# Performance work log

Hardware: AMD Instinct MI355X
Metric: run time of the kernel (lower is better)

## Reference

```python
import jax, jax.numpy as jnp
import numpy as np

U = 256      # lstm_unit / embedding_fc_unit
V = 100000   # word vocab
WD = 300     # word embedding dim
PD = 64      # pos embedding dim
AD = 64      # action embedding dim
P = 50       # pos vocab
NA = 164     # 4 + 4*dep_num actions
B, T, K, L, S, A, DQ = 64, 128, 4, 128, 64, 64, 32
FORGET_BIAS = 1.0


def lstm_step(x, c, h, W, b):
    z = jnp.concatenate([x, h], -1) @ W + b
    i, j, f, o = jnp.split(z, 4, -1)
    nc = c * jax.nn.sigmoid(f + FORGET_BIAS) + jax.nn.sigmoid(i) * jnp.tanh(j)
    nh = jnp.tanh(nc) * jax.nn.sigmoid(o)
    return nc, nh


def run_lstm(xs, length, W, b):
    # xs: [B, L, D]; TF dynamic_rnn semantics: state frozen and output zeroed past length.
    Bn, Ln, _ = xs.shape
    u = W.shape[1] // 4
    def step(carry, tx):
        c, h = carry
        t, x = tx
        nc, nh = lstm_step(x, c, h, W, b)
        m = (t < length)[:, None]
        return (jnp.where(m, nc, c), jnp.where(m, nh, h)), jnp.where(m, nh, 0.0)
    init = (jnp.zeros((Bn, u), xs.dtype), jnp.zeros((Bn, u), xs.dtype))
    (cf, hf), outs = jax.lax.scan(step, init, (jnp.arange(Ln), jnp.swapaxes(xs, 0, 1)))
    return jnp.swapaxes(outs, 0, 1), (cf, hf)


def reverse_seq(xs, length):
    # tf.reverse_sequence: reverse first `length` steps, leave the rest in place.
    Ln = xs.shape[1]
    t = jnp.arange(Ln)[None, :]
    rev = jnp.where(t < length[:, None], length[:, None] - 1 - t, t)
    return jnp.take_along_axis(xs, rev[:, :, None], axis=1)


def forward(tree_word_id, tree_pos_id, token_word_id, token_pos_id, history_action_id,
            buff_top_id, deque_word_id, deque_pos_id, deque_length, children_order,
            stack_order, stack_length, token_length, history_action_length,
            word_emb, pos_emb, act_emb, wd_W, wd_b, tree_W, tree_b,
            stack0_W, stack0_b, stack1_W, stack1_b,
            fw0_W, fw0_b, bw0_W, bw0_b, fw1_W, fw1_b, bw1_W, bw1_b,
            act0_W, act0_b, act1_W, act1_b, dq0_W, dq0_b, dq1_W, dq1_b,
            fin_W, fin_b):
    Bn = tree_word_id.shape[0]

    def embed(wid, pid):
        e = jnp.concatenate([word_emb[wid], pos_emb[pid]], -1)
        return jax.nn.relu(e @ wd_W + wd_b)

    tree_e = embed(tree_word_id, tree_pos_id)       # [B, T, U]
    token_e = embed(token_word_id, token_pos_id)    # [B, L, U]
    deque_e = embed(deque_word_id, deque_pos_id)    # [B, DQ, U]
    hist_e = act_emb[history_action_id]             # [B, A, AD]

    # ---- tree LSTM over children structure ----
    Tn = tree_e.shape[1]
    Kn = children_order.shape[2]
    batch_col = jnp.arange(Bn)[:, None]
    H0 = jnp.zeros((Tn + 1, Bn, U), tree_e.dtype)
    C0 = jnp.zeros((Tn + 1, Bn, U), tree_e.dtype)

    def body(carry, i):
        H, C = carry
        idx = children_order[:, i]            # [B, K] indices into slots 0..i
        h = H[idx, batch_col]                 # [B, K, U]
        c = C[idx, batch_col]
        x = tree_e[:, i]                      # [B, U]
        hj = h.sum(1)
        ijo = jnp.concatenate([x, hj], -1) @ tree_W[:, :3 * U] + tree_b[:3 * U]
        xk = jnp.broadcast_to(x[:, None, :], (Bn, Kn, x.shape[-1]))
        f = jnp.concatenate([xk, h], -1) @ tree_W[:, 3 * U:] + tree_b[3 * U:]   # [B, K, U]
        ig, jg, og = jnp.split(ijo, 3, -1)
        nc = (c * jax.nn.sigmoid(f + FORGET_BIAS)).sum(1) + jax.nn.sigmoid(ig) * jnp.tanh(jg)
        nh = jnp.tanh(nc) * jax.nn.sigmoid(og)
        return (H.at[i + 1].set(nh), C.at[i + 1].set(nc)), None

    (H, _), _ = jax.lax.scan(body, (H0, C0), jnp.arange(Tn))
    stack_embedded = H[stack_order, batch_col]      # [B, S, U]

    # ---- stack LSTM (2-layer) ----
    o0, _ = run_lstm(stack_embedded, stack_length, stack0_W, stack0_b)
    _, (_, stack_h) = run_lstm(o0, stack_length, stack1_W, stack1_b)

    # ---- buff bi-LSTM (2 stacked bidirectional layers) ----
    fw0_o, _ = run_lstm(token_e, token_length, fw0_W, fw0_b)
    bw0_o, _ = run_lstm(reverse_seq(token_e, token_length), token_length, bw0_W, bw0_b)
    bw0_o = reverse_seq(bw0_o, token_length)
    x1 = jnp.concatenate([fw0_o, bw0_o], -1)
    fw1_o, (_, fw1_h) = run_lstm(x1, token_length, fw1_W, fw1_b)
    bw1_o, _ = run_lstm(reverse_seq(x1, token_length), token_length, bw1_W, bw1_b)
    bw1_o = reverse_seq(bw1_o, token_length)
    bidx = jnp.arange(Bn)
    fw_top = fw1_o[bidx, buff_top_id]
    bw_top = bw1_o[bidx, buff_top_id]
    bw_bottom = bw1_o[bidx, token_length - 1]
    buff_out = jnp.concatenate([fw1_h - fw_top, bw_top - bw_bottom], -1)

    # ---- action LSTM (2-layer) ----
    a0, _ = run_lstm(hist_e, history_action_length, act0_W, act0_b)
    _, (_, act_h) = run_lstm(a0, history_action_length, act1_W, act1_b)

    # ---- deque LSTM (2-layer) ----
    d0, _ = run_lstm(deque_e, deque_length, dq0_W, dq0_b)
    _, (_, dq_h) = run_lstm(d0, deque_length, dq1_W, dq1_b)

    feat = jnp.concatenate([stack_h, buff_out, act_h, dq_h], -1)   # [B, 5U]
    return jax.nn.relu(feat @ fin_W + fin_b)


def setup_inputs():
    key = jax.random.key(0)
    ks = jax.random.split(key, 48)
    r = lambda i, shape: jax.random.normal(ks[i], shape, jnp.float32) * 0.05
    ri = lambda i, shape, hi: jax.random.randint(ks[i], shape, 0, hi)
    inp = {}
    inp['tree_word_id'] = ri(0, (B, T), V)
    inp['tree_pos_id'] = ri(1, (B, T), P)
    inp['token_word_id'] = ri(2, (B, L), V)
    inp['token_pos_id'] = ri(3, (B, L), P)
    inp['history_action_id'] = ri(4, (B, A), NA)
    inp['buff_top_id'] = ri(5, (B,), L // 2)
    inp['deque_word_id'] = ri(6, (B, DQ), V)
    inp['deque_pos_id'] = ri(7, (B, DQ), P)
    inp['deque_length'] = jax.random.randint(ks[8], (B,), 1, DQ + 1)
    co = ri(9, (B, T, K), T)
    # a node may only reference already-computed children slots (<= step index)
    inp['children_order'] = jnp.minimum(co, jnp.arange(T)[None, :, None])
    inp['stack_order'] = ri(10, (B, S), T + 1)
    inp['stack_length'] = jax.random.randint(ks[11], (B,), 1, S + 1)
    inp['token_length'] = jax.random.randint(ks[12], (B,), L // 2, L + 1)
    inp['history_action_length'] = jax.random.randint(ks[13], (B,), 1, A + 1)
    inp['word_emb'] = r(14, (V, WD))
    inp['pos_emb'] = r(15, (P, PD))
    inp['act_emb'] = r(16, (NA, AD))
    inp['wd_W'] = r(17, (WD + PD, U)); inp['wd_b'] = jnp.zeros((U,))
    inp['tree_W'] = r(18, (2 * U, 4 * U)); inp['tree_b'] = jnp.zeros((4 * U,))
    inp['stack0_W'] = r(19, (2 * U, 4 * U)); inp['stack0_b'] = jnp.zeros((4 * U,))
    inp['stack1_W'] = r(20, (2 * U, 4 * U)); inp['stack1_b'] = jnp.zeros((4 * U,))
    inp['fw0_W'] = r(21, (2 * U, 4 * U)); inp['fw0_b'] = jnp.zeros((4 * U,))
    inp['bw0_W'] = r(22, (2 * U, 4 * U)); inp['bw0_b'] = jnp.zeros((4 * U,))
    inp['fw1_W'] = r(23, (3 * U, 4 * U)); inp['fw1_b'] = jnp.zeros((4 * U,))
    inp['bw1_W'] = r(24, (3 * U, 4 * U)); inp['bw1_b'] = jnp.zeros((4 * U,))
    inp['act0_W'] = r(25, (AD + U, 4 * U)); inp['act0_b'] = jnp.zeros((4 * U,))
    inp['act1_W'] = r(26, (2 * U, 4 * U)); inp['act1_b'] = jnp.zeros((4 * U,))
    inp['dq0_W'] = r(27, (2 * U, 4 * U)); inp['dq0_b'] = jnp.zeros((4 * U,))
    inp['dq1_W'] = r(28, (2 * U, 4 * U)); inp['dq1_b'] = jnp.zeros((4 * U,))
    inp['fin_W'] = r(29, (5 * U, NA)); inp['fin_b'] = jnp.zeros((NA,))
    return inp


def reference(tree_word_id, tree_pos_id, token_word_id, token_pos_id, history_action_id,
              buff_top_id, deque_word_id, deque_pos_id, deque_length, children_order,
              stack_order, stack_length, token_length, history_action_length,
              word_emb, pos_emb, act_emb, wd_W, wd_b, tree_W, tree_b,
              stack0_W, stack0_b, stack1_W, stack1_b,
              fw0_W, fw0_b, bw0_W, bw0_b, fw1_W, fw1_b, bw1_W, bw1_b,
              act0_W, act0_b, act1_W, act1_b, dq0_W, dq0_b, dq1_W, dq1_b,
              fin_W, fin_b):
    return forward(tree_word_id, tree_pos_id, token_word_id, token_pos_id, history_action_id,
                   buff_top_id, deque_word_id, deque_pos_id, deque_length, children_order,
                   stack_order, stack_length, token_length, history_action_length,
                   word_emb, pos_emb, act_emb, wd_W, wd_b, tree_W, tree_b,
                   stack0_W, stack0_b, stack1_W, stack1_b,
                   fw0_W, fw0_b, bw0_W, bw0_b, fw1_W, fw1_b, bw1_W, bw1_b,
                   act0_W, act0_b, act1_W, act1_b, dq0_W, dq0_b, dq1_W, dq1_b,
                   fin_W, fin_b)
```

## Files before the change

### kernel.cpp

```cpp
#include <hip/hip_runtime.h>
#include <hip/hip_bf16.h>
#include <hip/hip_fp16.h>
#include <cstdint>

#define BB   64
#define TT   128
#define KK   4
#define LL   128
#define SS   64
#define AA   64
#define DQN  32
#define UU   256
#define NAOUT 164
#define WDIM 300
#define PDIM 64
#define ADIM 64

#define OFF_TREE 0
#define OFF_S0   512
#define OFF_S1   1024
#define OFF_FW0  1536
#define OFF_BW0  2048
#define OFF_FW1  2560
#define OFF_BW1  3328
// ... 313 lines not shown
        const float fsum = c0 * sigm(fx + f0) + c1 * sigm(fx + f1)
                         + c2 * sigm(fx + f2) + c3 * sigm(fx + f3);
        const float nc = fsum + sigm(zi) * tanhf(zj);
        const float nh = tanhf(nc) * sigm(zo);
        __syncthreads();
        H[((size_t)(i + 1) * BB + b) * UU + u] = nh;
        C[((size_t)(i + 1) * BB + b) * UU + u] = nc;
    }
}

template<bool F32>
__device__ void run_token_l0_f4(int b, const P& p, float* smem, bool is_bw) {
    const int u = threadIdx.x;
    float* s_xh = smem;
    const int len = p.token_length[b];
    const float4* __restrict__ Wp = p.pkf + (size_t)(is_bw ? OFF_BW0 : OFF_FW0) * 256 + u;
    const float4 bz = load_bias4<F32>(is_bw ? p.bw0_b : p.fw0_b, u);

    float c0 = 0.f;
    s_xh[256 + u] = 0.f;
    for (int t = 0; t < len; ++t) {
        const int row = is_bw ? (len - 1 - t) : t;
        s_xh[u] = bf2f(p.token_e[((size_t)b * LL + row) * UU + u]);
        __syncthreads();
        const float nh = lstm_step_f4<512>(Wp, bz, s_xh, c0);
        p.x1[((size_t)b * LL + row) * 512 + (is_bw ? 256 : 0) + u] = f2bf(nh);
        __syncthreads();
        s_xh[256 + u] = nh;
    }
}

template<bool F32>
__device__ void run_act_dq_f4(int b, const P& p, float* smem) {
    const int u = threadIdx.x;
    float* s_xh0 = smem;
    float* s_xh1 = smem + 512;

    {
        const int len = p.history_action_length[b];
        const float4* __restrict__ W0 = p.pkf + (size_t)OFF_ACT0 * 256 + u;
        const float4* __restrict__ W1 = p.pkf + (size_t)OFF_ACT1 * 256 + u;
        const float4 bz0 = load_bias4<F32>(p.act0_b, u);
        const float4 bz1 = load_bias4<F32>(p.act1_b, u);
        float ca0 = 0.f, ca1 = 0.f, h1last = 0.f;
        s_xh0[ADIM + u] = 0.f;
        s_xh1[256 + u]  = 0.f;
        for (int t = 0; t < len; ++t) {
            const int aid = p.history_action_id[b * AA + t];
            if (u < ADIM) s_xh0[u] = ld1<F32>(p.act_emb, (size_t)aid * ADIM + u);
            __syncthreads();
            const float nh0 = lstm_step_f4<320>(W0, bz0, s_xh0, ca0);
            __syncthreads();
            s_xh0[ADIM + u] = nh0;
            s_xh1[u]        = nh0;
            __syncthreads();
            const float nh1 = lstm_step_f4<512>(W1, bz1, s_xh1, ca1);
            __syncthreads();
            s_xh1[256 + u] = nh1;
            h1last = nh1;
        }
        p.act_h[b * UU + u] = h1last;
    }
    __syncthreads();
    {
        const int len = p.deque_length[b];
        const float4* __restrict__ W0 = p.pkf + (size_t)OFF_DQ0 * 256 + u;
        const float4* __restrict__ W1 = p.pkf + (size_t)OFF_DQ1 * 256 + u;
        const float4 bz0 = load_bias4<F32>(p.dq0_b, u);
        const float4 bz1 = load_bias4<F32>(p.dq1_b, u);
        float cd0 = 0.f, cd1 = 0.f, h1last = 0.f;
        s_xh0[256 + u] = 0.f;
        s_xh1[256 + u] = 0.f;
        for (int t = 0; t < len; ++t) {
            s_xh0[u] = bf2f(p.deque_e[((size_t)b * DQN + t) * UU + u]);
            __syncthreads();
            const float nh0 = lstm_step_f4<512>(W0, bz0, s_xh0, cd0);
            __syncthreads();
            s_xh0[256 + u] = nh0;
            s_xh1[u]       = nh0;
            __syncthreads();
            const float nh1 = lstm_step_f4<512>(W1, bz1, s_xh1, cd1);
            __syncthreads();
            s_xh1[256 + u] = nh1;
            h1last = nh1;
        }
        p.dq_h[b * UU + u] = h1last;
    }
}

__global__ __launch_bounds__(256) void phase1_fb_kernel(P p) {
    __shared__ __align__(16) float smem[1536];
    const bool f32 = (p.flag[0] == 1);
    const int chain = blockIdx.x & 3;
    const int b     = blockIdx.x >> 2;
    if (f32) {
        if (chain == 0)      run_tree_f4<true>(b, p, smem);
        else if (chain == 1) run_token_l0_f4<true>(b, p, smem, false);
        else if (chain == 2) run_token_l0_f4<true>(b, p, smem, true);
        else                 run_act_dq_f4<true>(b, p, smem);
    } else {
        if (chain == 0)      run_tree_f4<false>(b, p, smem);
        else if (chain == 1) run_token_l0_f4<false>(b, p, smem, false);
        else if (chain == 2) run_token_l0_f4<false>(b, p, smem, true);
        else                 run_act_dq_f4<false>(b, p, smem);
    }
}

template<bool F32>
__device__ void run_stack_f4(int b, const P& p, float* smem) {
    const int u = threadIdx.x;
    float* s_xh0 = smem;
    float* s_xh1 = smem + 512;
    const int len = p.stack_length[b];
    const float4* __restrict__ W0 = p.pkf + (size_t)OFF_S0 * 256 + u;
    const float4* __restrict__ W1 = p.pkf + (size_t)OFF_S1 * 256 + u;
    const float4 bz0 = load_bias4<F32>(p.stack0_b, u);
    const float4 bz1 = load_bias4<F32>(p.stack1_b, u);
    float cs0 = 0.f, cs1 = 0.f, h1last = 0.f;
    s_xh0[256 + u] = 0.f;
    s_xh1[256 + u] = 0.f;
    for (int t = 0; t < len; ++t) {
        const int so = p.stack_order[b * SS + t];
        s_xh0[u] = p.H[((size_t)so * BB + b) * UU + u];
        __syncthreads();
        const float nh0 = lstm_step_f4<512>(W0, bz0, s_xh0, cs0);
        __syncthreads();
        s_xh0[256 + u] = nh0;
        s_xh1[u]       = nh0;
        __syncthreads();
        const float nh1 = lstm_step_f4<512>(W1, bz1, s_xh1, cs1);
        __syncthreads();
        s_xh1[256 + u] = nh1;
        h1last = nh1;
    }
    p.stack_h[b * UU + u] = h1last;
}

template<bool F32>
__device__ void run_token_l1_f4(int b, const P& p, float* smem, bool is_bw) {
    const int u = threadIdx.x;
    float* s_xh = smem;
    const int len  = p.token_length[b];
    const int btop = p.buff_top_id[b];
    const float4* __restrict__ Wp = p.pkf + (size_t)(is_bw ? OFF_BW1 : OFF_FW1) * 256 + u;
    const float4 bz = load_bias4<F32>(is_bw ? p.bw1_b : p.fw1_b, u);

    float c1 = 0.f, hlast = 0.f;
    s_xh[512 + u] = 0.f;
    for (int t = 0; t < len; ++t) {
        const int row = is_bw ? (len - 1 - t) : t;
        const ushort_t* xr = p.x1 + ((size_t)b * LL + row) * 512;
        s_xh[u]       = bf2f(xr[u]);
        s_xh[256 + u] = bf2f(xr[256 + u]);
        __syncthreads();
        const float nh = lstm_step_f4<768>(Wp, bz, s_xh, c1);
        if (!is_bw) {
            if (t == btop) p.fw_top[b * UU + u] = nh;
        } else {
            if (t == 0)              p.bw_bottom[b * UU + u] = nh;
            if (t == len - 1 - btop) p.bw_top[b * UU + u]    = nh;
        }
        __syncthreads();
        s_xh[512 + u] = nh;
        hlast = nh;
    }
    if (!is_bw) p.fw1_h[b * UU + u] = hlast;
}

__global__ __launch_bounds__(256) void phase2_fb_kernel(P p) {
    __shared__ __align__(16) float smem[1024];
    const bool f32 = (p.flag[0] == 1);
    const int chain = blockIdx.x % 3;
    const int b     = blockIdx.x / 3;
    if (f32) {
        if (chain == 0)      run_stack_f4<true>(b, p, smem);
        else if (chain == 1) run_token_l1_f4<true>(b, p, smem, false);
        else                 run_token_l1_f4<true>(b, p, smem, true);
    } else {
        if (chain == 0)      run_stack_f4<false>(b, p, smem);
        else if (chain == 1) run_token_l1_f4<false>(b, p, smem, false);
        else                 run_token_l1_f4<false>(b, p, smem, true);
    }
}

template<bool F32, int R>
__device__ void xpre_compute(const void* __restrict__ W, const void* __restrict__ bias,
                             uint2* __restrict__ zx, int n0,
                             const float* __restrict__ s_xf, const ushort_t* __restrict__ s_xb) {
    const int u = threadIdx.x;
    const float4 bz = load_bias4<F32>(bias, u);
    for (int c = 0; c < 32; c += 8) {
        float4 acc[8];
        #pragma unroll
        for (int n = 0; n < 8; ++n) acc[n] = bz;
        for (int r0 = 0; r0 < R; r0 += 8) {
            float4 w[8];
            #pragma unroll
            for (int k = 0; k < 8; ++k) {
                const size_t ro = (size_t)(r0 + k) * 1024;
                w[k] = make_float4(ld1<F32>(W, ro + u),
                                   ld1<F32>(W, ro + 256 + u),
                                   ld1<F32>(W, ro + 512 + u),
                                   ld1<F32>(W, ro + 768 + u));
            }
            #pragma unroll
            for (int n = 0; n < 8; ++n) {
                float xv[8];
                #pragma unroll
                for (int k = 0; k < 8; ++k)
                    xv[k] = (R == 512) ? bf2f(s_xb[(size_t)(c + n) * 512 + r0 + k])
                                       : s_xf[(size_t)(c + n) * R + r0 + k];
                #pragma unroll
                for (int k = 0; k < 8; ++k) {
                    acc[n].x = fmaf(xv[k], w[k].x, acc[n].x);
                    acc[n].y = fmaf(xv[k], w[k].y, acc[n].y);
                    acc[n].z = fmaf(xv[k], w[k].z, acc[n].z);
                    acc[n].w = fmaf(xv[k], w[k].w, acc[n].w);
                }
            }
        }
        #pragma unroll
        for (int n = 0; n < 8; ++n) {
            uint2 v;
            v.x = pack2h(acc[n].x, acc[n].y);
            v.y = pack2h(acc[n].z, acc[n].w);
            zx[(size_t)(n0 + c + n) * 256 + u] = v;
        }
    }
}

template<bool F32, int STAGE>
__device__ void xpre_impl(const P& p, char* s_raw) {
    float*    s_xf = reinterpret_cast<float*>(s_raw);
    ushort_t* s_xb = reinterpret_cast<ushort_t*>(s_raw);
    const int blk = blockIdx.x;
    const int tid = threadIdx.x;

    const void* W; const void* bias; uint2* zx; int R; int kind; int n0;
    if (STAGE == 0) {
        if (blk < 256)      { W=p.fw0_W;  bias=p.fw0_b;  zx=p.zxA; R=256; kind=0; n0=blk*32; }
        else if (blk < 512) { W=p.bw0_W;  bias=p.bw0_b;  zx=p.zxB; R=256; kind=0; n0=(blk-256)*32; }
        else if (blk < 640) { W=p.act0_W; bias=p.act0_b; zx=p.zxC; R=64;  kind=3; n0=(blk-512)*32; }
        else                { W=p.dq0_W;  bias=p.dq0_b;  zx=p.zxD; R=256; kind=1; n0=(blk-640)*32; }
    } else if (STAGE == 1) {
        if (blk < 256)      { W=p.fw1_W;    bias=p.fw1_b;    zx=p.zxA; R=512; kind=2; n0=blk*32; }
        else if (blk < 512) { W=p.bw1_W;    bias=p.bw1_b;    zx=p.zxB; R=512; kind=2; n0=(blk-256)*32; }
        else if (blk < 640) { W=p.stack0_W; bias=p.stack0_b; zx=p.zxS; R=256; kind=4; n0=(blk-512)*32; }
        else if (blk < 768) { W=p.act1_W;   bias=p.act1_b;   zx=p.zxC; R=256; kind=5; n0=(blk-640)*32; }
        else                { W=p.dq1_W;    bias=p.dq1_b;    zx=p.zxD; R=256; kind=6; n0=(blk-768)*32; }
    } else {
        W=p.stack1_W; bias=p.stack1_b; zx=p.zxS; R=256; kind=7; n0=blk*32;
    }

    if (kind == 0 || kind == 1) {
        const ushort_t* src = (kind == 0 ? p.token_e : p.deque_e) + (size_t)n0 * 256;
        for (int i = tid; i < 32 * 256; i += 256) s_xf[i] = bf2f(src[i]);
    } else if (kind == 2) {
        const ushort_t* src = p.x1 + (size_t)n0 * 512;
        for (int i = tid; i < 32 * 512; i += 256) s_xb[i] = src[i];
    } else if (kind == 3) {
        const int b = n0 >> 6, t0 = n0 & 63;
        for (int i = tid; i < 32 * 64; i += 256) {
            const int t = t0 + (i >> 6), r = i & 63;
            int aid = p.history_action_id[b * AA + t];
            aid = aid < 0 ? 0 : (aid > NAOUT - 1 ? NAOUT - 1 : aid);
            s_xf[i] = ld1<F32>(p.act_emb, (size_t)aid * ADIM + r);
        }
    } else if (kind == 4) {
        const int b = n0 >> 6, t0 = n0 & 63;
        for (int i = tid; i < 32 * 256; i += 256) {
            const int t = t0 + (i >> 8), r = i & 255;
            int so = p.stack_order[b * SS + t];
            so = so < 0 ? 0 : (so > TT ? TT : so);
            s_xf[i] = p.H[((size_t)so * BB + b) * UU + r];
        }
    } else {
        const float* src = (kind == 5 ? p.a0_seq : kind == 6 ? p.d0_seq : p.s0_seq)
                         + (size_t)n0 * 256;
        for (int i = tid; i < 32 * 256; i += 256) s_xf[i] = src[i];
    }
    __syncthreads();

    if (R == 512)      xpre_compute<F32, 512>(W, bias, zx, n0, s_xf, s_xb);
    else if (R == 256) xpre_compute<F32, 256>(W, bias, zx, n0, s_xf, s_xb);
    else               xpre_compute<F32, 64 >(W, bias, zx, n0, s_xf, s_xb);
}

__global__ __launch_bounds__(256) void xpre0_kernel(P p) {
    __shared__ __align__(16) char s_raw[32768];
    if (p.flag[0] == 1) xpre_impl<true, 0>(p, s_raw);
    else                xpre_impl<false, 0>(p, s_raw);
}
__global__ __launch_bounds__(256) void xpre1_kernel(P p) {
    __shared__ __align__(16) char s_raw[32768];
    if (p.flag[0] == 1) xpre_impl<true, 1>(p, s_raw);
    else                xpre_impl<false, 1>(p, s_raw);
}
__global__ __launch_bounds__(256) void xpre2_kernel(P p) {
    __shared__ __align__(16) char s_raw[32768];
    if (p.flag[0] == 1) xpre_impl<true, 2>(p, s_raw);
    else                xpre_impl<false, 2>(p, s_raw);
}

template<bool F32>
__device__ void p1_impl(const P& p, float* smem) {
    const int chain = blockIdx.x >> 6;
    const int b     = blockIdx.x & 63;
    if (chain == 0) { run_tree_f4<F32>(b, p, smem); return; }

    const int u = threadIdx.x;
    float* s_h = smem;
    float c = 0.f;
    s_h[u] = 0.f;
    __syncthreads();

    if (chain == 1 || chain == 2) {
        const bool bw = (chain == 2);
        const int len = p.token_length[b];
        const float4* __restrict__ Wh = p.pkf + (size_t)(bw ? PKH_BW0 : PKH_FW0) * 256 + u;
        const uint2* zx = bw ? p.zxB : p.zxA;
        for (int t = 0; t < len; ++t) {
            const int row = bw ? (len - 1 - t) : t;
            const float4 bz = zx_load(zx, (size_t)b * LL + row, u);
            const float nh = lstm_step_f4<256>(Wh, bz, s_h, c);
            p.x1[((size_t)b * LL + row) * 512 + (bw ? 256 : 0) + u] = f2bf(nh);
            __syncthreads();
            s_h[u] = nh;
            __syncthreads();
        }
    } else if (chain == 3) {
        const int len = p.history_action_length[b];
        const float4* __restrict__ Wh = p.pkf + (size_t)PKH_ACT0 * 256 + u;
        for (int t = 0; t < len; ++t) {
            const float4 bz = zx_load(p.zxC, (size_t)b * AA + t, u);
            const float nh = lstm_step_f4<256>(Wh, bz, s_h, c);
            p.a0_seq[((size_t)b * AA + t) * UU + u] = nh;
            __syncthreads();
            s_h[u] = nh;
            __syncthreads();
        }
    } else {
        const int len = p.deque_length[b];
        const float4* __restrict__ Wh = p.pkf + (size_t)PKH_DQ0 * 256 + u;
        for (int t = 0; t < len; ++t) {
            const float4 bz = zx_load(p.zxD, (size_t)b * DQN + t, u);
            const float nh = lstm_step_f4<256>(Wh, bz, s_h, c);
            p.d0_seq[((size_t)b * DQN + t) * UU + u] = nh;
            __syncthreads();
            s_h[u] = nh;
            __syncthreads();
        }
    }
}

__global__ __launch_bounds__(256) void p1_kernel(P p) {
    __shared__ __align__(16) float smem[1536];
    if (p.flag[0] == 1) p1_impl<true>(p, smem);
    else                p1_impl<false>(p, smem);
}

template<bool F32>
__device__ void p2_impl(const P& p, float* smem) {
    const int chain = blockIdx.x >> 6;
    const int b     = blockIdx.x & 63;
    const int u = threadIdx.x;
    float* s_h = smem;
    float c = 0.f;
    s_h[u] = 0.f;
    __syncthreads();

    if (chain == 0) {
        const int len  = p.token_length[b];
        const int btop = p.buff_top_id[b];
        const float4* __restrict__ Wh = p.pkf + (size_t)PKH_FW1 * 256 + u;
        float hlast = 0.f;
        for (int t = 0; t < len; ++t) {
            const float4 bz = zx_load(p.zxA, (size_t)b * LL + t, u);
            const float nh = lstm_step_f4<256>(Wh, bz, s_h, c);
            if (t == btop) p.fw_top[b * UU + u] = nh;
            __syncthreads();
            s_h[u] = nh;
            __syncthreads();
            hlast = nh;
        }
        p.fw1_h[b * UU + u] = hlast;
    } else if (chain == 1) {
        const int len  = p.token_length[b];
        const int btop = p.buff_top_id[b];
        const float4* __restrict__ Wh = p.pkf + (size_t)PKH_BW1 * 256 + u;
        for (int t = 0; t < len; ++t) {
            const int row = len - 1 - t;
            const float4 bz = zx_load(p.zxB, (size_t)b * LL + row, u);
            const float nh = lstm_step_f4<256>(Wh, bz, s_h, c);
            if (t == 0)              p.bw_bottom[b * UU + u] = nh;
            if (t == len - 1 - btop) p.bw_top[b * UU + u]    = nh;
            __syncthreads();
            s_h[u] = nh;
            __syncthreads();
        }
    } else if (chain == 2) {
        const int len = p.stack_length[b];
        const float4* __restrict__ Wh = p.pkf + (size_t)PKH_S0 * 256 + u;
        for (int t = 0; t < len; ++t) {
            const float4 bz = zx_load(p.zxS, (size_t)b * SS + t, u);
            const float nh = lstm_step_f4<256>(Wh, bz, s_h, c);
            p.s0_seq[((size_t)b * SS + t) * UU + u] = nh;
            __syncthreads();
            s_h[u] = nh;
            __syncthreads();
        }
    } else if (chain == 3) {
        const int len = p.history_action_length[b];
        const float4* __restrict__ Wh = p.pkf + (size_t)PKH_ACT1 * 256 + u;
        float hlast = 0.f;
        for (int t = 0; t < len; ++t) {
            const float4 bz = zx_load(p.zxC, (size_t)b * AA + t, u);
            const float nh = lstm_step_f4<256>(Wh, bz, s_h, c);
            __syncthreads();
            s_h[u] = nh;
            __syncthreads();
            hlast = nh;
        }
        p.act_h[b * UU + u] = hlast;
    } else {
        const int len = p.deque_length[b];
        const float4* __restrict__ Wh = p.pkf + (size_t)PKH_DQ1 * 256 + u;
        float hlast = 0.f;
        for (int t = 0; t < len; ++t) {
            const float4 bz = zx_load(p.zxD, (size_t)b * DQN + t, u);
            const float nh = lstm_step_f4<256>(Wh, bz, s_h, c);
            __syncthreads();
            s_h[u] = nh;
            __syncthreads();
            hlast = nh;
        }
        p.dq_h[b * UU + u] = hlast;
    }
}

__global__ __launch_bounds__(256) void p2_kernel(P p) {
    __shared__ __align__(16) float smem[256];
    if (p.flag[0] == 1) p2_impl<true>(p, smem);
    else                p2_impl<false>(p, smem);
}

template<bool F32>
__device__ void p3_impl(const P& p, float* smem) {
    const int b = blockIdx.x;
    const int u = threadIdx.x;
    float* s_h = smem;
    float c = 0.f;
    s_h[u] = 0.f;
    __syncthreads();
    const int len = p.stack_length[b];
    const float4* __restrict__ Wh = p.pkf + (size_t)PKH_S1 * 256 + u;
    float hlast = 0.f;
    for (int t = 0; t < len; ++t) {
        const float4 bz = zx_load(p.zxS, (size_t)b * SS + t, u);
        const float nh = lstm_step_f4<256>(Wh, bz, s_h, c);
        __syncthreads();
        s_h[u] = nh;
        __syncthreads();
        hlast = nh;
    }
    p.stack_h[b * UU + u] = hlast;
}

__global__ __launch_bounds__(256) void p3_kernel(P p) {
    __shared__ __align__(16) float smem[256];
    if (p.flag[0] == 1) p3_impl<true>(p, smem);
    else                p3_impl<false>(p, smem);
}

template<bool F32>
__device__ __forceinline__ void st_out(void* out, int i, float v) {
    if constexpr (F32) reinterpret_cast<float*>(out)[i] = v;
    else               reinterpret_cast<__hip_bfloat16*>(out)[i] = __float2bfloat16(v);
}

template<bool F32>
__device__ void final_impl(const P& p, void* out, float* s_f) {
    const int b = blockIdx.x;
    const int u = threadIdx.x;
    s_f[u]        = p.stack_h[b * UU + u];
    s_f[256 + u]  = p.fw1_h[b * UU + u] - p.fw_top[b * UU + u];
    s_f[512 + u]  = p.bw_top[b * UU + u] - p.bw_bottom[b * UU + u];
    s_f[768 + u]  = p.act_h[b * UU + u];
    s_f[1024 + u] = p.dq_h[b * UU + u];
    __syncthreads();
    if (u < NAOUT) {
        float acc = ld1<F32>(p.fin_b, u);
        for (int r = 0; r < 1280; ++r)
            acc = fmaf(s_f[r], ld1<F32>(p.fin_W, (size_t)r * NAOUT + u), acc);
        acc = fmaxf(acc, 0.f);
        st_out<F32>(out, b * NAOUT + u, acc);
    }
    if (b == 0 && u == 0) {
        const uint_t POIS = 0xAAAAAAAAu;
        const uint_t* te = reinterpret_cast<const uint_t*>(p.tree_e);
        const uint_t* x1 = reinterpret_cast<const uint_t*>(p.x1);
        const uint_t* sh = reinterpret_cast<const uint_t*>(p.stack_h);
        bool te_p = true, x1_p = true;
        for (int i = 0; i < 8; ++i) { te_p &= (te[i] == POIS); x1_p &= (x1[i] == POIS); }
        bool sh_p = (sh[0] == POIS) && (sh[1] == POIS);
        float sent = 0.f;
        if (te_p)      sent = 3000.f;
        else if (x1_p) sent = 4000.f;
        else if (sh_p) sent = 5000.f;
        else if (*reinterpret_cast<const uint_t*>(p.flag) == POIS) sent = 6000.f;
        if (sent > 0.f) st_out<F32>(out, 0, sent);
    }
}

__global__ __launch_bounds__(256) void final_kernel(P p, void* out) {
    __shared__ __align__(16) float s_f[1280];
    if (p.flag[0] == 1) final_impl<true>(p, out, s_f);
    else                final_impl<false>(p, out, s_f);
}

extern "C" void kernel_launch(void* const* d_in, const int* in_sizes, int n_in,
                              void* d_out, int out_size, void* d_ws, size_t ws_size,
                              hipStream_t stream) {
    if (n_in != 43) {
        sentinel_kernel<<<1, 64, 0, stream>>>(d_out, 9000.f + (float)n_in);
        return;
    }
    if (out_size != NAOUT * BB) {
        sentinel_kernel<<<1, 64, 0, stream>>>(d_out, 8000.f);
        return;
    }

    P p;
    p.tree_word_id          = (const int*)d_in[0];
    p.tree_pos_id           = (const int*)d_in[1];
    p.token_word_id         = (const int*)d_in[2];
    p.token_pos_id          = (const int*)d_in[3];
    p.history_action_id     = (const int*)d_in[4];
    p.buff_top_id           = (const int*)d_in[5];
    p.deque_word_id         = (const int*)d_in[6];
    p.deque_pos_id          = (const int*)d_in[7];
    p.deque_length          = (const int*)d_in[8];
    p.children_order        = (const int*)d_in[9];
    p.stack_order           = (const int*)d_in[10];
    p.stack_length          = (const int*)d_in[11];
    p.token_length          = (const int*)d_in[12];
    p.history_action_length = (const int*)d_in[13];
    p.word_emb = d_in[14];
    p.pos_emb  = d_in[15];
    p.act_emb  = d_in[16];
    p.wd_W     = d_in[17];
    p.wd_b     = d_in[18];
    p.tree_W   = d_in[19];
    p.tree_b   = d_in[20];
    p.stack0_W = d_in[21];
    p.stack0_b = d_in[22];
    p.stack1_W = d_in[23];
    p.stack1_b = d_in[24];
    p.fw0_W    = d_in[25];
    p.fw0_b    = d_in[26];
    p.bw0_W    = d_in[27];
    p.bw0_b    = d_in[28];
    p.fw1_W    = d_in[29];
    p.fw1_b    = d_in[30];
    p.bw1_W    = d_in[31];
    p.bw1_b    = d_in[32];
    p.act0_W   = d_in[33];
    p.act0_b   = d_in[34];
    p.act1_W   = d_in[35];
    p.act1_b   = d_in[36];
    p.dq0_W    = d_in[37];
    p.dq0_b    = d_in[38];
    p.dq1_W    = d_in[39];
    p.dq1_b    = d_in[40];
    p.fin_W    = d_in[41];
    p.fin_b    = d_in[42];

    char* base = (char*)d_ws;

    size_t off = 0;
    p.flag = (int*)(base + off);           off += 256;
    p.stack_h   = (float*)(base + off);    off += (size_t)BB * UU * 4;
    p.fw1_h     = (float*)(base + off);    off += (size_t)BB * UU * 4;
    p.fw_top    = (float*)(base + off);    off += (size_t)BB * UU * 4;
    p.bw_top    = (float*)(base + off);    off += (size_t)BB * UU * 4;
    p.bw_bottom = (float*)(base + off);    off += (size_t)BB * UU * 4;
    p.act_h     = (float*)(base + off);    off += (size_t)BB * UU * 4;
    p.dq_h      = (float*)(base + off);    off += (size_t)BB * UU * 4;
    p.tree_e  = (float*)(base + off);      off += (size_t)BB * TT * UU * 4;
    p.token_e = (ushort_t*)(base + off);   off += (size_t)BB * LL * UU * 2;
    p.deque_e = (ushort_t*)(base + off);   off += (size_t)BB * DQN * UU * 2;
    p.x1      = (ushort_t*)(base + off);   off += (size_t)BB * LL * 512 * 2;
    p.a0_seq  = (float*)(base + off);      off += (size_t)BB * AA * UU * 4;
    p.d0_seq  = (float*)(base + off);      off += (size_t)BB * DQN * UU * 4;
    p.s0_seq  = (float*)(base + off);      off += (size_t)BB * SS * UU * 4;
    p.H       = (float*)(base + off);      off += (size_t)(TT + 1) * BB * UU * 4;
    p.C       = (float*)(base + off);      off += (size_t)(TT + 1) * BB * UU * 4;
    p.zxA     = (uint2*)(base + off);      off += (size_t)BB * LL * UU * 8;
    p.zxB     = (uint2*)(base + off);      off += (size_t)BB * LL * UU * 8;
    p.zxC     = (uint2*)(base + off);      off += (size_t)BB * AA * UU * 8;
    p.zxD     = (uint2*)(base + off);      off += (size_t)BB * DQN * UU * 8;
    p.zxS     = (uint2*)(base + off);      off += (size_t)BB * SS * UU * 8;
    p.pkf     = (float4*)(base + off);     off += (size_t)PK_ROWS_B * 256 * 16;
    const size_t planB_size = off;

    if (ws_size >= planB_size) {
        detect_kernel<<<1, 64, 0, stream>>>((const uint_t*)d_in[14], p.flag);
        pack_h_kernel<<<dim3(PK_ROWS_B), dim3(256), 0, stream>>>(p);
        embed_kernel<<<dim3(BB * TT + BB * LL + BB * DQN), dim3(256), 0, stream>>>(p);
        xpre0_kernel<<<dim3(704), dim3(256), 0, stream>>>(p);
        p1_kernel<<<dim3(5 * BB), dim3(256), 0, stream>>>(p);
        xpre1_kernel<<<dim3(832), dim3(256), 0, stream>>>(p);
        p2_kernel<<<dim3(5 * BB), dim3(256), 0, stream>>>(p);
        xpre2_kernel<<<dim3(128), dim3(256), 0, stream>>>(p);
        p3_kernel<<<dim3(BB), dim3(256), 0, stream>>>(p);
        final_kernel<<<dim3(BB), dim3(256), 0, stream>>>(p, d_out);
        return;
    }

    off = 0;
    p.flag = (int*)(base + off);           off += 16;
    p.stack_h   = (float*)(base + off);    off += (size_t)BB * UU * 4;
    p.fw1_h     = (float*)(base + off);    off += (size_t)BB * UU * 4;
    p.fw_top    = (float*)(base + off);    off += (size_t)BB * UU * 4;
    p.bw_top    = (float*)(base + off);    off += (size_t)BB * UU * 4;
    p.bw_bottom = (float*)(base + off);    off += (size_t)BB * UU * 4;
    p.act_h     = (float*)(base + off);    off += (size_t)BB * UU * 4;
    p.dq_h      = (float*)(base + off);    off += (size_t)BB * UU * 4;
    p.tree_e  = (float*)(base + off);      off += (size_t)BB * TT * UU * 4;
    p.token_e = (ushort_t*)(base + off);   off += (size_t)BB * LL * UU * 2;
    p.deque_e = (ushort_t*)(base + off);   off += (size_t)BB * DQN * UU * 2;
    p.x1      = (ushort_t*)(base + off);   off += (size_t)BB * LL * 512 * 2;
    p.H       = (float*)(base + off);      off += (size_t)(TT + 1) * BB * UU * 4;
    p.C       = (float*)(base + off);      off += (size_t)(TT + 1) * BB * UU * 4;
    p.pkf     = (float4*)(base + off);     off += (size_t)PK_ROWS_FB * 256 * 16;
    p.a0_seq = p.d0_seq = p.s0_seq = (float*)base;
    p.zxA = p.zxB = p.zxC = p.zxD = p.zxS = (uint2*)base;

    if (ws_size < off) {
        sentinel_kernel<<<1, 64, 0, stream>>>(d_out, 7000.f + (float)(ws_size >> 20));
        return;
    }

    detect_kernel<<<1, 64, 0, stream>>>((const uint_t*)d_in[14], p.flag);
    pack_fb_kernel<<<dim3(PK_ROWS_FB), dim3(256), 0, stream>>>(p);
    embed_kernel<<<dim3(BB * TT + BB * LL + BB * DQN), dim3(256), 0, stream>>>(p);
    phase1_fb_kernel<<<dim3(4 * BB), dim3(256), 0, stream>>>(p);
    phase2_fb_kernel<<<dim3(3 * BB), dim3(256), 0, stream>>>(p);
    final_kernel<<<dim3(BB), dim3(256), 0, stream>>>(p, d_out);
}
```

Before: 6.336 ms.

## Split recurrent LSTM matvec across four thread groups with 1024-thread blocks

The sequential LSTM recurrence kernels (tree, bidirectional, action, deque, stack chains) now use 1024 threads per block. Each group of 256 threads computes a 64-row (or 128-row for the tree) slice of the hidden-state matvec, and the partial sums are reduced through shared memory before the gate math. The goal is to shorten the per-step latency of the serial recurrence by spreading the weight loads and FMAs over four times as many threads. In exchange it adds a partial-sum shared buffer, an extra reduction step and barriers across 16 wavefronts, and it raises register and LDS pressure per block.

```diff
diff --git a/kernel.cpp b/kernel.cpp
--- a/kernel.cpp
+++ b/kernel.cpp
@@ -639,16 +639,209 @@
     else                xpre_impl<false, 2>(p, s_raw);
 }
 
+
+__device__ __forceinline__ float4 part64(const float4* __restrict__ W_u, int base,
+                                         const float* __restrict__ s_h) {
+    float4 acc = make_float4(0.f, 0.f, 0.f, 0.f);
+    for (int r0 = 0; r0 < 64; r0 += 8) {
+        float4 w[8];
+        #pragma unroll
+        for (int k = 0; k < 8; ++k) w[k] = W_u[(size_t)(base + r0 + k) * 256];
+        __builtin_amdgcn_sched_barrier(0);
+        #pragma unroll
+        for (int q = 0; q < 2; ++q) {
+            const float4 x4 = *reinterpret_cast<const float4*>(s_h + base + r0 + 4 * q);
+            const float xv[4] = {x4.x, x4.y, x4.z, x4.w};
+            #pragma unroll
+            for (int j = 0; j < 4; ++j) {
+                const float4 wv = w[4 * q + j];
+                acc.x = fmaf(xv[j], wv.x, acc.x);
+                acc.y = fmaf(xv[j], wv.y, acc.y);
+                acc.z = fmaf(xv[j], wv.z, acc.z);
+                acc.w = fmaf(xv[j], wv.w, acc.w);
+            }
+        }
+    }
+    return acc;
+}
+
+__device__ __forceinline__ float hstep(const float4* __restrict__ W_u,
+                                       const uint2* __restrict__ zx, size_t n,
+                                       float* s_h, float* s_pt,
+                                       float& c, int u, int rq) {
+    float4 bz = make_float4(0.f, 0.f, 0.f, 0.f);
+    if (rq == 0) bz = zx_load(zx, n, u);
+    const float4 acc = part64(W_u, rq << 6, s_h);
+    *reinterpret_cast<float4*>(s_pt + (((rq << 8) + u) << 2)) = acc;
+    __syncthreads();
+    float nh = 0.f;
+    if (rq == 0) {
+        const float4 P0 = *reinterpret_cast<const float4*>(s_pt + ((u)        << 2));
+        const float4 P1 = *reinterpret_cast<const float4*>(s_pt + ((256 + u)  << 2));
+        const float4 P2 = *reinterpret_cast<const float4*>(s_pt + ((512 + u)  << 2));
+        const float4 P3 = *reinterpret_cast<const float4*>(s_pt + ((768 + u)  << 2));
+        const float zi = bz.x + P0.x + P1.x + P2.x + P3.x;
+        const float zj = bz.y + P0.y + P1.y + P2.y + P3.y;
+        const float zf = bz.z + P0.z + P1.z + P2.z + P3.z;
+        const float zo = bz.w + P0.w + P1.w + P2.w + P3.w;
+        const float nc = c * sigm(zf) + sigm(zi) * tanhf(zj);
+        c = nc;
+        nh = tanhf(nc) * sigm(zo);
+    }
+    return nh;
+}
+
+template<bool F32>
+__device__ void run_tree_1024(int b, const P& p, float* smem) {
+    const int t = threadIdx.x;
+    const int u = t & 255, rq = t >> 8;
+    float* s_x  = smem;
+    float* s_hk = smem + 256;
+    float* s_pt = smem + 1280;
+    float* H = p.H;
+    float* C = p.C;
+    if (rq == 0) {
+        H[(size_t)b * UU + u] = 0.f;
+        C[(size_t)b * UU + u] = 0.f;
+    }
+    const float4* __restrict__ Wt = p.pkf + u;
+    const float4* __restrict__ Wh = Wt + (size_t)256 * 256;
+    const float bi = ld1<F32>(p.tree_b, u);
+    const float bj = ld1<F32>(p.tree_b, 256 + u);
+    const float bo = ld1<F32>(p.tree_b, 512 + u);
+    const float bf = ld1<F32>(p.tree_b, 768 + u) + 1.0f;
+    __syncthreads();
+
+    for (int i = 0; i < TT; ++i) {
+        const int* co = p.children_order + ((size_t)b * TT + i) * KK;
+        float c0 = 0.f, c1 = 0.f, c2 = 0.f, c3 = 0.f;
+        if (rq == 0) {
+            const int i0 = co[0], i1 = co[1], i2 = co[2], i3 = co[3];
+            const float h0 = H[((size_t)i0 * BB + b) * UU + u];
+            const float h1 = H[((size_t)i1 * BB + b) * UU + u];
+            const float h2 = H[((size_t)i2 * BB + b) * UU + u];
+            const float h3 = H[((size_t)i3 * BB + b) * UU + u];
+            c0 = C[((size_t)i0 * BB + b) * UU + u];
+            c1 = C[((size_t)i1 * BB + b) * UU + u];
+            c2 = C[((size_t)i2 * BB + b) * UU + u];
+            c3 = C[((size_t)i3 * BB + b) * UU + u];
+            s_hk[u]       = h0;
+            s_hk[256 + u] = h1;
+            s_hk[512 + u] = h2;
+            s_hk[768 + u] = h3;
+        } else if (rq == 1) {
+            s_x[u] = p.tree_e[((size_t)b * TT + i) * UU + u];
+        }
+        __syncthreads();
+
+        float p0, p1, p2, p3, p4, p5, p6, p7;
+        if (rq < 2) {
+            float zi = 0.f, zj = 0.f, zo = 0.f, fx = 0.f;
+            const int base = rq << 7;
+            for (int r0 = 0; r0 < 128; r0 += 8) {
+                float4 w[8];
+                #pragma unroll
+                for (int k = 0; k < 8; ++k) w[k] = Wt[(size_t)(base + r0 + k) * 256];
+                __builtin_amdgcn_sched_barrier(0);
+                #pragma unroll
+                for (int q = 0; q < 2; ++q) {
+                    const float4 x4 = *reinterpret_cast<const float4*>(s_x + base + r0 + 4 * q);
+                    const float xv[4] = {x4.x, x4.y, x4.z, x4.w};
+                    #pragma unroll
+                    for (int j = 0; j < 4; ++j) {
+                        const float4 wv = w[4 * q + j];
+                        zi = fmaf(xv[j], wv.x, zi);
+                        zj = fmaf(xv[j], wv.y, zj);
+                        zo = fmaf(xv[j], wv.z, zo);
+                        fx = fmaf(xv[j], wv.w, fx);
+                    }
+                }
+            }
+            p0 = zi; p1 = zj; p2 = zo; p3 = fx;
+            p4 = 0.f; p5 = 0.f; p6 = 0.f; p7 = 0.f;
+        } else {
+            float zi = 0.f, zj = 0.f, zo = 0.f;
+            float f0 = 0.f, f1 = 0.f, f2 = 0.f, f3 = 0.f;
+            const int base = (rq - 2) << 7;
+            for (int r0 = 0; r0 < 128; r0 += 8) {
+                float4 w[8];
+                #pragma unroll
+                for (int k = 0; k < 8; ++k) w[k] = Wh[(size_t)(base + r0 + k) * 256];
+                __builtin_amdgcn_sched_barrier(0);
+                #pragma unroll
+                for (int q = 0; q < 2; ++q) {
+                    const int r = base + r0 + 4 * q;
+                    const float4 a0 = *reinterpret_cast<const float4*>(s_hk + r);
+                    const float4 a1 = *reinterpret_cast<const float4*>(s_hk + 256 + r);
+                    const float4 a2 = *reinterpret_cast<const float4*>(s_hk + 512 + r);
+                    const float4 a3 = *reinterpret_cast<const float4*>(s_hk + 768 + r);
+                    const float hj[4] = {a0.x + a1.x + a2.x + a3.x,
+                                         a0.y + a1.y + a2.y + a3.y,
+                                         a0.z + a1.z + a2.z + a3.z,
+                                         a0.w + a1.w + a2.w + a3.w};
+                    const float k0[4] = {a0.x, a0.y, a0.z, a0.w};
+                    const float k1[4] = {a1.x, a1.y, a1.z, a1.w};
+                    const float k2[4] = {a2.x, a2.y, a2.z, a2.w};
+                    const float k3[4] = {a3.x, a3.y, a3.z, a3.w};
+                    #pragma unroll
+                    for (int j = 0; j < 4; ++j) {
+                        const float4 wv = w[4 * q + j];
+                        zi = fmaf(hj[j], wv.x, zi);
+                        zj = fmaf(hj[j], wv.y, zj);
+                        zo = fmaf(hj[j], wv.z, zo);
+                        f0 = fmaf(k0[j], wv.w, f0);
+                        f1 = fmaf(k1[j], wv.w, f1);
+                        f2 = fmaf(k2[j], wv.w, f2);
+                        f3 = fmaf(k3[j], wv.w, f3);
+                    }
+                }
+            }
+            p0 = zi; p1 = zj; p2 = zo; p3 = 0.f;
+            p4 = f0; p5 = f1; p6 = f2; p7 = f3;
+        }
+        float* pt = s_pt + (((rq << 8) + u) << 3);
+        *reinterpret_cast<float4*>(pt)     = make_float4(p0, p1, p2, p3);
+        *reinterpret_cast<float4*>(pt + 4) = make_float4(p4, p5, p6, p7);
+        __syncthreads();
+        if (rq == 0) {
+            float4 A[4], Bv[4];
+            #pragma unroll
+            for (int g = 0; g < 4; ++g) {
+                const float* q_ = s_pt + (((g << 8) + u) << 3);
+                A[g]  = *reinterpret_cast<const float4*>(q_);
+                Bv[g] = *reinterpret_cast<const float4*>(q_ + 4);
+            }
+            const float zi = bi + A[0].x + A[1].x + A[2].x + A[3].x;
+            const float zj = bj + A[0].y + A[1].y + A[2].y + A[3].y;
+            const float zo = bo + A[0].z + A[1].z + A[2].z + A[3].z;
+            const float fx = bf + A[0].w + A[1].w + A[2].w + A[3].w;
+            const float f0 = Bv[0].x + Bv[1].x + Bv[2].x + Bv[3].x;
+            const float f1 = Bv[0].y + Bv[1].y + Bv[2].y + Bv[3].y;
+            const float f2 = Bv[0].z + Bv[1].z + Bv[2].z + Bv[3].z;
+            const float f3 = Bv[0].w + Bv[1].w + Bv[2].w + Bv[3].w;
+            const float fsum = c0 * sigm(fx + f0) + c1 * sigm(fx + f1)
+                             + c2 * sigm(fx + f2) + c3 * sigm(fx + f3);
+            const float nc = fsum + sigm(zi) * tanhf(zj);
+            const float nh = tanhf(nc) * sigm(zo);
+            H[((size_t)(i + 1) * BB + b) * UU + u] = nh;
+            C[((size_t)(i + 1) * BB + b) * UU + u] = nc;
+        }
+        __syncthreads();
+    }
+}
+
 template<bool F32>
 __device__ void p1_impl(const P& p, float* smem) {
     const int chain = blockIdx.x >> 6;
     const int b     = blockIdx.x & 63;
-    if (chain == 0) { run_tree_f4<F32>(b, p, smem); return; }
-
-    const int u = threadIdx.x;
-    float* s_h = smem;
+    if (chain == 0) { run_tree_1024<F32>(b, p, smem); return; }
+
+    const int t = threadIdx.x;
+    const int u = t & 255, rq = t >> 8;
+    float* s_h  = smem;
+    float* s_pt = smem + 256;
     float c = 0.f;
-    s_h[u] = 0.f;
+    if (rq == 0) s_h[u] = 0.f;
     __syncthreads();
 
     if (chain == 1 || chain == 2) {
@@ -656,42 +849,42 @@
         const int len = p.token_length[b];
         const float4* __restrict__ Wh = p.pkf + (size_t)(bw ? PKH_BW0 : PKH_FW0) * 256 + u;
         const uint2* zx = bw ? p.zxB : p.zxA;
-        for (int t = 0; t < len; ++t) {
-            const int row = bw ? (len - 1 - t) : t;
-            const float4 bz = zx_load(zx, (size_t)b * LL + row, u);
-            const float nh = lstm_step_f4<256>(Wh, bz, s_h, c);
-            p.x1[((size_t)b * LL + row) * 512 + (bw ? 256 : 0) + u] = f2bf(nh);
-            __syncthreads();
-            s_h[u] = nh;
+        for (int tt = 0; tt < len; ++tt) {
+            const int row = bw ? (len - 1 - tt) : tt;
+            const float nh = hstep(Wh, zx, (size_t)b * LL + row, s_h, s_pt, c, u, rq);
+            if (rq == 0) {
+                p.x1[((size_t)b * LL + row) * 512 + (bw ? 256 : 0) + u] = f2bf(nh);
+                s_h[u] = nh;
+            }
             __syncthreads();
         }
     } else if (chain == 3) {
         const int len = p.history_action_length[b];
         const float4* __restrict__ Wh = p.pkf + (size_t)PKH_ACT0 * 256 + u;
-        for (int t = 0; t < len; ++t) {
-            const float4 bz = zx_load(p.zxC, (size_t)b * AA + t, u);
-            const float nh = lstm_step_f4<256>(Wh, bz, s_h, c);
-            p.a0_seq[((size_t)b * AA + t) * UU + u] = nh;
-            __syncthreads();
-            s_h[u] = nh;
+        for (int tt = 0; tt < len; ++tt) {
+            const float nh = hstep(Wh, p.zxC, (size_t)b * AA + tt, s_h, s_pt, c, u, rq);
+            if (rq == 0) {
+                p.a0_seq[((size_t)b * AA + tt) * UU + u] = nh;
+                s_h[u] = nh;
+            }
             __syncthreads();
         }
     } else {
         const int len = p.deque_length[b];
         const float4* __restrict__ Wh = p.pkf + (size_t)PKH_DQ0 * 256 + u;
-        for (int t = 0; t < len; ++t) {
-            const float4 bz = zx_load(p.zxD, (size_t)b * DQN + t, u);
-            const float nh = lstm_step_f4<256>(Wh, bz, s_h, c);
-            p.d0_seq[((size_t)b * DQN + t) * UU + u] = nh;
-            __syncthreads();
-            s_h[u] = nh;
-            __syncthreads();
-        }
-    }
-}
-
-__global__ __launch_bounds__(256) void p1_kernel(P p) {
-    __shared__ __align__(16) float smem[1536];
+        for (int tt = 0; tt < len; ++tt) {
+            const float nh = hstep(Wh, p.zxD, (size_t)b * DQN + tt, s_h, s_pt, c, u, rq);
+            if (rq == 0) {
+                p.d0_seq[((size_t)b * DQN + tt) * UU + u] = nh;
+                s_h[u] = nh;
+            }
+            __syncthreads();
+        }
+    }
+}
+
+__global__ __launch_bounds__(1024) void p1_kernel(P p) {
+    __shared__ __align__(16) float smem[9472];
     if (p.flag[0] == 1) p1_impl<true>(p, smem);
     else                p1_impl<false>(p, smem);
 }
@@ -700,10 +893,12 @@
 __device__ void p2_impl(const P& p, float* smem) {
     const int chain = blockIdx.x >> 6;
     const int b     = blockIdx.x & 63;
-    const int u = threadIdx.x;
-    float* s_h = smem;
+    const int t = threadIdx.x;
+    const int u = t & 255, rq = t >> 8;
+    float* s_h  = smem;
+    float* s_pt = smem + 256;
     float c = 0.f;
-    s_h[u] = 0.f;
+    if (rq == 0) s_h[u] = 0.f;
     __syncthreads();
 
     if (chain == 0) {
@@ -711,72 +906,66 @@
         const int btop = p.buff_top_id[b];
         const float4* __restrict__ Wh = p.pkf + (size_t)PKH_FW1 * 256 + u;
         float hlast = 0.f;
-        for (int t = 0; t < len; ++t) {
-            const float4 bz = zx_load(p.zxA, (size_t)b * LL + t, u);
-            const float nh = lstm_step_f4<256>(Wh, bz, s_h, c);
-            if (t == btop) p.fw_top[b * UU + u] = nh;
-            __syncthreads();
-            s_h[u] = nh;
-            __syncthreads();
-            hlast = nh;
-        }
-        p.fw1_h[b * UU + u] = hlast;
+        for (int tt = 0; tt < len; ++tt) {
+            const float nh = hstep(Wh, p.zxA, (size_t)b * LL + tt, s_h, s_pt, c, u, rq);
+            if (rq == 0) {
+                if (tt == btop) p.fw_top[b * UU + u] = nh;
+                s_h[u] = nh;
+                hlast = nh;
+            }
+            __syncthreads();
+        }
+        if (rq == 0) p.fw1_h[b * UU + u] = hlast;
     } else if (chain == 1) {
         const int len  = p.token_length[b];
         const int btop = p.buff_top_id[b];
         const float4* __restrict__ Wh = p.pkf + (size_t)PKH_BW1 * 256 + u;
-        for (int t = 0; t < len; ++t) {
-            const int row = len - 1 - t;
-            const float4 bz = zx_load(p.zxB, (size_t)b * LL + row, u);
-            const float nh = lstm_step_f4<256>(Wh, bz, s_h, c);
-            if (t == 0)              p.bw_bottom[b * UU + u] = nh;
-            if (t == len - 1 - btop) p.bw_top[b * UU + u]    = nh;
-            __syncthreads();
-            s_h[u] = nh;
+        for (int tt = 0; tt < len; ++tt) {
+            const int row = len - 1 - tt;
+            const float nh = hstep(Wh, p.zxB, (size_t)b * LL + row, s_h, s_pt, c, u, rq);
+            if (rq == 0) {
+                if (tt == 0)              p.bw_bottom[b * UU + u] = nh;
+                if (tt == len - 1 - btop) p.bw_top[b * UU + u]    = nh;
+                s_h[u] = nh;
+            }
             __syncthreads();
         }
     } else if (chain == 2) {
         const int len = p.stack_length[b];
         const float4* __restrict__ Wh = p.pkf + (size_t)PKH_S0 * 256 + u;
-        for (int t = 0; t < len; ++t) {
-            const float4 bz = zx_load(p.zxS, (size_t)b * SS + t, u);
-            const float nh = lstm_step_f4<256>(Wh, bz, s_h, c);
-            p.s0_seq[((size_t)b * SS + t) * UU + u] = nh;
-            __syncthreads();
-            s_h[u] = nh;
+        for (int tt = 0; tt < len; ++tt) {
+            const float nh = hstep(Wh, p.zxS, (size_t)b * SS + tt, s_h, s_pt, c, u, rq);
+            if (rq == 0) {
+                p.s0_seq[((size_t)b * SS + tt) * UU + u] = nh;
+                s_h[u] = nh;
+            }
             __syncthreads();
         }
     } else if (chain == 3) {
         const int len = p.history_action_length[b];
         const float4* __restrict__ Wh = p.pkf + (size_t)PKH_ACT1 * 256 + u;
         float hlast = 0.f;
-        for (int t = 0; t < len; ++t) {
-            const float4 bz = zx_load(p.zxC, (size_t)b * AA + t, u);
-            const float nh = lstm_step_f4<256>(Wh, bz, s_h, c);
-            __syncthreads();
-            s_h[u] = nh;
-            __syncthreads();
-            hlast = nh;
-        }
-        p.act_h[b * UU + u] = hlast;
+        for (int tt = 0; tt < len; ++tt) {
+            const float nh = hstep(Wh, p.zxC, (size_t)b * AA + tt, s_h, s_pt, c, u, rq);
+            if (rq == 0) { s_h[u] = nh; hlast = nh; }
+            __syncthreads();
+        }
+        if (rq == 0) p.act_h[b * UU + u] = hlast;
     } else {
         const int len = p.deque_length[b];
         const float4* __restrict__ Wh = p.pkf + (size_t)PKH_DQ1 * 256 + u;
         float hlast = 0.f;
-        for (int t = 0; t < len; ++t) {
-            const float4 bz = zx_load(p.zxD, (size_t)b * DQN + t, u);
-            const float nh = lstm_step_f4<256>(Wh, bz, s_h, c);
-            __syncthreads();
-            s_h[u] = nh;
-            __syncthreads();
-            hlast = nh;
-        }
-        p.dq_h[b * UU + u] = hlast;
-    }
-}
-
-__global__ __launch_bounds__(256) void p2_kernel(P p) {
-    __shared__ __align__(16) float smem[256];
+        for (int tt = 0; tt < len; ++tt) {
+            const float nh = hstep(Wh, p.zxD, (size_t)b * DQN + tt, s_h, s_pt, c, u, rq);
+            if (rq == 0) { s_h[u] = nh; hlast = nh; }
+            __syncthreads();
+        }
+        if (rq == 0) p.dq_h[b * UU + u] = hlast;
+    }
+}
+
+__global__ __launch_bounds__(1024) void p2_kernel(P p) {
+    __shared__ __align__(16) float smem[4352];
     if (p.flag[0] == 1) p2_impl<true>(p, smem);
     else                p2_impl<false>(p, smem);
 }
@@ -784,27 +973,26 @@
 template<bool F32>
 __device__ void p3_impl(const P& p, float* smem) {
     const int b = blockIdx.x;
-    const int u = threadIdx.x;
-    float* s_h = smem;
+    const int t = threadIdx.x;
+    const int u = t & 255, rq = t >> 8;
+    float* s_h  = smem;
+    float* s_pt = smem + 256;
     float c = 0.f;
-    s_h[u] = 0.f;
+    if (rq == 0) s_h[u] = 0.f;
     __syncthreads();
     const int len = p.stack_length[b];
     const float4* __restrict__ Wh = p.pkf + (size_t)PKH_S1 * 256 + u;
     float hlast = 0.f;
-    for (int t = 0; t < len; ++t) {
-        const float4 bz = zx_load(p.zxS, (size_t)b * SS + t, u);
-        const float nh = lstm_step_f4<256>(Wh, bz, s_h, c);
-        __syncthreads();
-        s_h[u] = nh;
-        __syncthreads();
-        hlast = nh;
-    }
-    p.stack_h[b * UU + u] = hlast;
-}
-
-__global__ __launch_bounds__(256) void p3_kernel(P p) {
-    __shared__ __align__(16) float smem[256];
+    for (int tt = 0; tt < len; ++tt) {
+        const float nh = hstep(Wh, p.zxS, (size_t)b * SS + tt, s_h, s_pt, c, u, rq);
+        if (rq == 0) { s_h[u] = nh; hlast = nh; }
+        __syncthreads();
+    }
+    if (rq == 0) p.stack_h[b * UU + u] = hlast;
+}
+
+__global__ __launch_bounds__(1024) void p3_kernel(P p) {
+    __shared__ __align__(16) float smem[4352];
     if (p.flag[0] == 1) p3_impl<true>(p, smem);
     else                p3_impl<false>(p, smem);
 }
@@ -945,11 +1133,11 @@
         pack_h_kernel<<<dim3(PK_ROWS_B), dim3(256), 0, stream>>>(p);
         embed_kernel<<<dim3(BB * TT + BB * LL + BB * DQN), dim3(256), 0, stream>>>(p);
         xpre0_kernel<<<dim3(704), dim3(256), 0, stream>>>(p);
-        p1_kernel<<<dim3(5 * BB), dim3(256), 0, stream>>>(p);
+        p1_kernel<<<dim3(5 * BB), dim3(1024), 0, stream>>>(p);
         xpre1_kernel<<<dim3(832), dim3(256), 0, stream>>>(p);
-        p2_kernel<<<dim3(5 * BB), dim3(256), 0, stream>>>(p);
+        p2_kernel<<<dim3(5 * BB), dim3(1024), 0, stream>>>(p);
         xpre2_kernel<<<dim3(128), dim3(256), 0, stream>>>(p);
-        p3_kernel<<<dim3(BB), dim3(256), 0, stream>>>(p);
+        p3_kernel<<<dim3(BB), dim3(1024), 0, stream>>>(p);
         final_kernel<<<dim3(BB), dim3(256), 0, stream>>>(p, d_out);
         return;
     }
```

Result: slower. 10.43 ms (+64.6%).
